# Optimization experiments

Hardware: AMD Instinct MI355X
Metric: run time of the kernel (lower is better)

The kernel has to match this reference:

```python
import jax, jax.numpy as jnp
import numpy as np

B, T, D = 4, 2048, 1024
E = 16            # routed experts
S = 2             # shared experts
MOE_TOPK = 2
COSINE_LAMBDA = 0.1


def setup_inputs() -> dict:
    key = jax.random.key(0)
    k_x, k_g, k_sh, k_rt = jax.random.split(key, 4)
    x = jax.random.normal(k_x, (B, T, D), dtype=jnp.float32)
    gate_w = jax.random.normal(k_g, (E, D), dtype=jnp.float32) * 0.02
    gate_b = jnp.zeros((E,), dtype=jnp.float32)
    shared_experts = jax.random.normal(k_sh, (S, D), dtype=jnp.float32) * 0.1
    routed_experts = jax.random.normal(k_rt, (E, D), dtype=jnp.float32) * 0.1
    return {"x": x, "gate_w": gate_w, "gate_b": gate_b,
            "shared_experts": shared_experts, "routed_experts": routed_experts}


def reference(x, gate_w, gate_b, shared_experts, routed_experts):
    b, t, d = x.shape
    n = b * t
    hidden = x.reshape(n, d)                                   # [N, D]

    # ---- router ----
    logits = hidden @ gate_w.T + gate_b                        # [N, E]
    probs = jax.nn.softmax(logits, axis=-1)                    # stable (shift-invariant)
    topk_vals, topk_idx = jax.lax.top_k(probs, MOE_TOPK)       # [N, K]
    if MOE_TOPK == 1:
        weights = jnp.ones_like(topk_vals)
    else:
        weights = topk_vals / jnp.clip(topk_vals.sum(-1, keepdims=True), 1e-6)

    # ---- shared experts (always active): sum_e hidden * w_e ----
    shared_sum = hidden * shared_experts.sum(0)                # [N, D]

    # ---- dense all-expert elementwise scale (as in original) ----
    routed_outs = hidden[None, :, :] * routed_experts[:, None, :]   # [E, N, D]

    # ---- diversity loss: cosine sim between flattened expert outputs ----
    flat = routed_outs.reshape(E, -1)                          # [E, N*D]
    norms = jnp.maximum(jnp.linalg.norm(flat, axis=1, keepdims=True), 1e-8)
    normed = flat / norms
    sim = jnp.clip(normed @ normed.T, -1.0, 1.0)               # [E, E]
    mask = 1.0 - jnp.eye(E, dtype=sim.dtype)
    div_loss = (sim * mask).sum() / max(E * (E - 1), 1) * COSINE_LAMBDA

    # ---- top-k gather + weighted combine ----
    routed_nd = routed_outs.transpose(1, 0, 2)                 # [N, E, D]
    sel = jnp.take_along_axis(routed_nd, topk_idx[:, :, None], axis=1)  # [N, K, D]
    dyn_sum = (sel * weights[:, :, None]).sum(axis=1)          # [N, D]

    out = (shared_sum + dyn_sum).reshape(b, t, d)
    return out, div_loss
```

## Files before the change

kernel.cpp:

```cpp
#include <hip/hip_runtime.h>

#define NTOK 8192
#define DDIM 1024
#define NEXP 16
#define NPAIR 136
#define XROW 1032
#define NBLK 2048
#define NRED 64

#define WS_GWT  0
#define WS_SLOT 16384
#define WS_GP   (WS_SLOT + NBLK * DDIM)

__global__ __launch_bounds__(256) void moe_prep(
    const float* __restrict__ gate_w,
    float* __restrict__ ws)
{
    const int gid = blockIdx.x * 256 + threadIdx.x;
    const int e = gid & 15;
    const int d4 = gid >> 4;
    const float4* gw4 = (const float4*)gate_w;
    float4* gwT4 = (float4*)(ws + WS_GWT);
    gwT4[d4 * 16 + e] = gw4[e * 256 + d4];
}

__global__ __launch_bounds__(256, 8) void moe_fused(
    const float* __restrict__ x,
    const float* __restrict__ gate_b,
    const float* __restrict__ sh,
    const float* __restrict__ re,
    float* __restrict__ out,
    float* __restrict__ ws)
{
    __shared__ __align__(16) float xt[4][XROW];

    const int t = threadIdx.x;
    const int b = blockIdx.x;
    const float4* gwT4 = (const float4*)(ws + WS_GWT);

    float4 ss = make_float4(0.f, 0.f, 0.f, 0.f);
    {
        const float4* x4 = (const float4*)x + (size_t)b * 1024;
        #pragma unroll
        for (int i = 0; i < 4; ++i) {
            float4 v = x4[i * 256 + t];
            *(float4*)&xt[i][4 * t] = v;
            ss.x = fmaf(v.x, v.x, ss.x);
            ss.y = fmaf(v.y, v.y, ss.y);
            ss.z = fmaf(v.z, v.z, ss.z);
            ss.w = fmaf(v.w, v.w, ss.w);
        }
    }
    __syncthreads();

    const int lane = t & 63;
    const int wv = t >> 6;
    const int e = lane & 15;
    const int qr = lane >> 4;

    const float* xrow = &xt[wv][qr * 256];
    const float4* gt = gwT4 + qr * 64 * 16;
    float4 a4 = make_float4(0.f, 0.f, 0.f, 0.f);
    #pragma unroll 8
    for (int i = 0; i < 64; ++i) {
        float4 xv = *(const float4*)(xrow + 4 * i);
        float4 gv = gt[i * 16 + e];
        a4.x = fmaf(xv.x, gv.x, a4.x);
        a4.y = fmaf(xv.y, gv.y, a4.y);
        a4.z = fmaf(xv.z, gv.z, a4.z);
        a4.w = fmaf(xv.w, gv.w, a4.w);
    }
    float acc = (a4.x + a4.y) + (a4.z + a4.w);
    acc += __shfl_xor(acc, 16, 64);
    acc += __shfl_xor(acc, 32, 64);
    acc += gate_b[e];

    float v0 = -3.0e38f, v1 = -3.0e38f;
    int i0 = 0, i1 = 0;
    const int base = lane & 48;
    #pragma unroll
    for (int j = 0; j < NEXP; ++j) {
        float lv = __shfl(acc, base + j, 64);
        if (lv > v0)      { v1 = v0; i1 = i0; v0 = lv; i0 = j; }
        else if (lv > v1) { v1 = lv; i1 = j; }
    }
    float ex = __expf(v1 - v0);
    float w0 = 1.f / (1.f + ex);
    float w1 = ex * w0;

    float4 shs[4];
    {
        const float4* s0 = (const float4*)sh;
        const float4* s1 = (const float4*)(sh + DDIM);
        #pragma unroll
        for (int j = 0; j < 4; ++j) {
            float4 p = s0[lane + 64 * j];
            float4 s = s1[lane + 64 * j];
            shs[j] = make_float4(p.x + s.x, p.y + s.y, p.z + s.z, p.w + s.w);
        }
    }

    {
        const float4* xr = (const float4*)&xt[wv][0];
        const float4* r0 = (const float4*)(re + (size_t)i0 * DDIM);
        const float4* r1 = (const float4*)(re + (size_t)i1 * DDIM);
        float4* o = (float4*)(out + ((size_t)b * 4 + wv) * DDIM);
        #pragma unroll
        for (int j = 0; j < 4; ++j) {
            const int idx = lane + 64 * j;
            float4 xv = xr[idx];
            float4 b0 = r0[idx];
            float4 b1 = r1[idx];
            float4 r;
            r.x = xv.x * (shs[j].x + w0 * b0.x + w1 * b1.x);
            r.y = xv.y * (shs[j].y + w0 * b0.y + w1 * b1.y);
            r.z = xv.z * (shs[j].z + w0 * b0.z + w1 * b1.z);
            r.w = xv.w * (shs[j].w + w0 * b0.w + w1 * b1.w);
            o[idx] = r;
        }
    }

    *(float4*)(ws + WS_SLOT + (size_t)b * DDIM + 4 * t) = ss;
}

__global__ __launch_bounds__(256) void moe_xred_gram(
    const float* __restrict__ re,
    float* __restrict__ ws)
{
    __shared__ float4 s4[64][4];
    __shared__ float s_loc[16];
    __shared__ float reT[16][16];

    const int t = threadIdx.x;
    const int j = blockIdx.x;
    const int c = t & 3;
    const int r = t >> 2;

    {
        const float4* sl4 = (const float4*)(ws + WS_SLOT);
        const size_t colbase = (size_t)4 * j + c;
        float4 acc = make_float4(0.f, 0.f, 0.f, 0.f);
        #pragma unroll 8
        for (int k = 0; k < 32; ++k) {
            float4 v = sl4[(size_t)(r + 64 * k) * 256 + colbase];
            acc.x += v.x; acc.y += v.y; acc.z += v.z; acc.w += v.w;
        }
        s4[r][c] = acc;
    }
    {
        const int e = t >> 4, dd = t & 15;
        reT[dd][e] = re[(size_t)e * DDIM + 16 * j + dd];
    }
    __syncthreads();

    if (t < 4) {
        float4 a = s4[0][t];
        for (int rr = 1; rr < 64; ++rr) {
            float4 v = s4[rr][t];
            a.x += v.x; a.y += v.y; a.z += v.z; a.w += v.w;
        }
        s_loc[4 * t + 0] = a.x;
        s_loc[4 * t + 1] = a.y;
        s_loc[4 * t + 2] = a.z;
        s_loc[4 * t + 3] = a.w;
    }
    __syncthreads();

    if (t < NPAIR) {
        int pe = 0, rem = t;
        while (rem >= NEXP - pe) { rem -= NEXP - pe; ++pe; }
        const int pf = pe + rem;
        float a = 0.f;
        #pragma unroll
        for (int dd = 0; dd < 16; ++dd)
            a += s_loc[dd] * reT[dd][pe] * reT[dd][pf];
        (ws + WS_GP)[j * NPAIR + t] = a;
    }
}

__global__ __launch_bounds__(192) void moe_final(
    const float* __restrict__ ws,
    float* __restrict__ div_out)
{
    __shared__ float G[NPAIR];
    __shared__ float nr[NEXP];
    __shared__ float lsum;
    const int t = threadIdx.x;

    if (t == 0) lsum = 0.f;
    if (t < NPAIR) {
        const float* gp = ws + WS_GP;
        float g = 0.f;
        #pragma unroll 8
        for (int jj = 0; jj < NRED; ++jj) g += gp[jj * NPAIR + t];
        G[t] = g;
    }
    __syncthreads();
    if (t < NEXP) {
        int idx = t * NEXP - (t * (t - 1)) / 2;
        nr[t] = fmaxf(sqrtf(G[idx]), 1e-8f);
    }
    __syncthreads();
    if (t < NPAIR) {
        int pe = 0, rem = t;
        while (rem >= NEXP - pe) { rem -= NEXP - pe; ++pe; }
        const int pf = pe + rem;
        if (pe != pf) {
            float sim = G[t] / (nr[pe] * nr[pf]);
            sim = fminf(1.f, fmaxf(-1.f, sim));
            atomicAdd(&lsum, 2.f * sim);
        }
    }
    __syncthreads();
    if (t == 0) *div_out = lsum / (float)(NEXP * (NEXP - 1)) * 0.1f;
}

extern "C" void kernel_launch(void* const* d_in, const int* in_sizes, int n_in,
                              void* d_out, int out_size, void* d_ws, size_t ws_size,
                              hipStream_t stream) {
    const float* x  = (const float*)d_in[0];
    const float* gw = (const float*)d_in[1];
    const float* gb = (const float*)d_in[2];
    const float* sh = (const float*)d_in[3];
    const float* re = (const float*)d_in[4];
    float* out = (float*)d_out;
    float* ws = (float*)d_ws;

    moe_prep<<<16, 256, 0, stream>>>(gw, ws);
    moe_fused<<<NBLK, 256, 0, stream>>>(x, gb, sh, re, out, ws);
    moe_xred_gram<<<NRED, 256, 0, stream>>>(re, ws);
    moe_final<<<1, 192, 0, stream>>>(ws, out + (size_t)NTOK * DDIM);
}
```

Before: 130.0 us.

## Fuse final reduction into gram kernel via last-block counter and pad LDS rows

Removes the separate single-block final kernel: each gram block atomically stores its partials, increments a counter, and the last block reads all partials under an acquire fence and computes the diversity loss. The shared-memory x tile is padded per quarter row, adding 8 floats after each 256, to reduce LDS bank conflicts in the router dot product. The sum-of-squares store is also moved before the barrier. This saves one kernel launch but adds an atomic counter and fence, and relies on the prep kernel resetting the counter on every call.

Measured after the change: 141.7 us. +9.0%, slower.

```diff
diff --git a/kernel.cpp b/kernel.cpp
--- a/kernel.cpp
+++ b/kernel.cpp
@@ -4,13 +4,14 @@
 #define DDIM 1024
 #define NEXP 16
 #define NPAIR 136
-#define XROW 1032
+#define QPAD 264
 #define NBLK 2048
 #define NRED 64
 
 #define WS_GWT  0
 #define WS_SLOT 16384
 #define WS_GP   (WS_SLOT + NBLK * DDIM)
+#define WS_CNT  (WS_GP + NRED * NPAIR)
 
 __global__ __launch_bounds__(256) void moe_prep(
     const float* __restrict__ gate_w,
@@ -22,6 +23,7 @@
     const float4* gw4 = (const float4*)gate_w;
     float4* gwT4 = (float4*)(ws + WS_GWT);
     gwT4[d4 * 16 + e] = gw4[e * 256 + d4];
+    if (gid == 0) ((int*)ws)[WS_CNT] = 0;
 }
 
 __global__ __launch_bounds__(256, 8) void moe_fused(
@@ -32,7 +34,7 @@
     float* __restrict__ out,
     float* __restrict__ ws)
 {
-    __shared__ __align__(16) float xt[4][XROW];
+    __shared__ __align__(16) float xt[4][4 * QPAD];
 
     const int t = threadIdx.x;
     const int b = blockIdx.x;
@@ -41,16 +43,18 @@
     float4 ss = make_float4(0.f, 0.f, 0.f, 0.f);
     {
         const float4* x4 = (const float4*)x + (size_t)b * 1024;
+        const int dst = 4 * t + 8 * (t >> 6);
         #pragma unroll
         for (int i = 0; i < 4; ++i) {
             float4 v = x4[i * 256 + t];
-            *(float4*)&xt[i][4 * t] = v;
+            *(float4*)&xt[i][dst] = v;
             ss.x = fmaf(v.x, v.x, ss.x);
             ss.y = fmaf(v.y, v.y, ss.y);
             ss.z = fmaf(v.z, v.z, ss.z);
             ss.w = fmaf(v.w, v.w, ss.w);
         }
     }
+    *(float4*)(ws + WS_SLOT + (size_t)b * DDIM + 4 * t) = ss;
     __syncthreads();
 
     const int lane = t & 63;
@@ -58,7 +62,7 @@
     const int e = lane & 15;
     const int qr = lane >> 4;
 
-    const float* xrow = &xt[wv][qr * 256];
+    const float* xrow = &xt[wv][qr * QPAD];
     const float4* gt = gwT4 + qr * 64 * 16;
     float4 a4 = make_float4(0.f, 0.f, 0.f, 0.f);
     #pragma unroll 8
@@ -101,14 +105,13 @@
     }
 
     {
-        const float4* xr = (const float4*)&xt[wv][0];
         const float4* r0 = (const float4*)(re + (size_t)i0 * DDIM);
         const float4* r1 = (const float4*)(re + (size_t)i1 * DDIM);
         float4* o = (float4*)(out + ((size_t)b * 4 + wv) * DDIM);
         #pragma unroll
         for (int j = 0; j < 4; ++j) {
             const int idx = lane + 64 * j;
-            float4 xv = xr[idx];
+            float4 xv = ((const float4*)&xt[wv][j * QPAD])[lane];
             float4 b0 = r0[idx];
             float4 b1 = r1[idx];
             float4 r;
@@ -119,22 +122,26 @@
             o[idx] = r;
         }
     }
-
-    *(float4*)(ws + WS_SLOT + (size_t)b * DDIM + 4 * t) = ss;
 }
 
 __global__ __launch_bounds__(256) void moe_xred_gram(
     const float* __restrict__ re,
-    float* __restrict__ ws)
+    float* __restrict__ ws,
+    float* __restrict__ div_out)
 {
     __shared__ float4 s4[64][4];
     __shared__ float s_loc[16];
     __shared__ float reT[16][16];
+    __shared__ float Gs[NPAIR];
+    __shared__ float nr[NEXP];
+    __shared__ float lsum;
+    __shared__ int   role;
 
     const int t = threadIdx.x;
     const int j = blockIdx.x;
     const int c = t & 3;
     const int r = t >> 2;
+    int* cnt = (int*)ws + WS_CNT;
 
     {
         const float4* sl4 = (const float4*)(ws + WS_SLOT);
@@ -174,18 +181,18 @@
         #pragma unroll
         for (int dd = 0; dd < 16; ++dd)
             a += s_loc[dd] * reT[dd][pe] * reT[dd][pf];
-        (ws + WS_GP)[j * NPAIR + t] = a;
-    }
-}
-
-__global__ __launch_bounds__(192) void moe_final(
-    const float* __restrict__ ws,
-    float* __restrict__ div_out)
-{
-    __shared__ float G[NPAIR];
-    __shared__ float nr[NEXP];
-    __shared__ float lsum;
-    const int t = threadIdx.x;
+        __hip_atomic_store(ws + WS_GP + j * NPAIR + t, a,
+                           __ATOMIC_RELAXED, __HIP_MEMORY_SCOPE_AGENT);
+    }
+
+    __syncthreads();
+    if (t == 0) {
+        int k = atomicAdd(cnt, 1);
+        role = (k == NRED - 1);
+    }
+    __syncthreads();
+    if (!role) return;
+    __builtin_amdgcn_fence(__ATOMIC_ACQUIRE, "agent");
 
     if (t == 0) lsum = 0.f;
     if (t < NPAIR) {
@@ -193,12 +200,12 @@
         float g = 0.f;
         #pragma unroll 8
         for (int jj = 0; jj < NRED; ++jj) g += gp[jj * NPAIR + t];
-        G[t] = g;
+        Gs[t] = g;
     }
     __syncthreads();
     if (t < NEXP) {
         int idx = t * NEXP - (t * (t - 1)) / 2;
-        nr[t] = fmaxf(sqrtf(G[idx]), 1e-8f);
+        nr[t] = fmaxf(sqrtf(Gs[idx]), 1e-8f);
     }
     __syncthreads();
     if (t < NPAIR) {
@@ -206,7 +213,7 @@
         while (rem >= NEXP - pe) { rem -= NEXP - pe; ++pe; }
         const int pf = pe + rem;
         if (pe != pf) {
-            float sim = G[t] / (nr[pe] * nr[pf]);
+            float sim = Gs[t] / (nr[pe] * nr[pf]);
             sim = fminf(1.f, fmaxf(-1.f, sim));
             atomicAdd(&lsum, 2.f * sim);
         }
@@ -228,6 +235,5 @@
 
     moe_prep<<<16, 256, 0, stream>>>(gw, ws);
     moe_fused<<<NBLK, 256, 0, stream>>>(x, gb, sh, re, out, ws);
-    moe_xred_gram<<<NRED, 256, 0, stream>>>(re, ws);
-    moe_final<<<1, 192, 0, stream>>>(ws, out + (size_t)NTOK * DDIM);
-}
+    moe_xred_gram<<<NRED, 256, 0, stream>>>(re, ws, out + (size_t)NTOK * DDIM);
+}
```

## Restructure router GEMV to reuse gate weights across four tokens and drop transpose kernel

Applied to the files above, without the earlier changes.

The separate gate-weight transpose kernel is removed. Each wave now reads gate_w rows directly and applies each loaded weight vector to four tokens, so the four waves split the D dimension. Partial logits are combined through a small shared-memory array and an extra barrier. The x tile in shared memory gets a padded layout with staggered iteration order to reduce bank conflicts. The cost is the extra sync and LDS round trip, plus more registers for four accumulators.

Result: slower. 134.4 us (+3.4%).

```diff
diff --git a/kernel.cpp b/kernel.cpp
--- a/kernel.cpp
+++ b/kernel.cpp
@@ -4,47 +4,36 @@
 #define DDIM 1024
 #define NEXP 16
 #define NPAIR 136
-#define XROW 1032
+#define QPAD 264
 #define NBLK 2048
 #define NRED 64
 
-#define WS_GWT  0
-#define WS_SLOT 16384
-#define WS_GP   (WS_SLOT + NBLK * DDIM)
-
-__global__ __launch_bounds__(256) void moe_prep(
-    const float* __restrict__ gate_w,
-    float* __restrict__ ws)
-{
-    const int gid = blockIdx.x * 256 + threadIdx.x;
-    const int e = gid & 15;
-    const int d4 = gid >> 4;
-    const float4* gw4 = (const float4*)gate_w;
-    float4* gwT4 = (float4*)(ws + WS_GWT);
-    gwT4[d4 * 16 + e] = gw4[e * 256 + d4];
-}
+#define WS_SLOT 0
+#define WS_GP   (NBLK * DDIM)
 
 __global__ __launch_bounds__(256, 8) void moe_fused(
     const float* __restrict__ x,
+    const float* __restrict__ gate_w,
     const float* __restrict__ gate_b,
     const float* __restrict__ sh,
     const float* __restrict__ re,
     float* __restrict__ out,
     float* __restrict__ ws)
 {
-    __shared__ __align__(16) float xt[4][XROW];
+    __shared__ __align__(16) float xt[4][4 * QPAD];
+    __shared__ float lg[4][4][16];
 
     const int t = threadIdx.x;
     const int b = blockIdx.x;
-    const float4* gwT4 = (const float4*)(ws + WS_GWT);
 
     float4 ss = make_float4(0.f, 0.f, 0.f, 0.f);
     {
         const float4* x4 = (const float4*)x + (size_t)b * 1024;
+        const int dst = 4 * t + 8 * (t >> 6);
         #pragma unroll
         for (int i = 0; i < 4; ++i) {
             float4 v = x4[i * 256 + t];
-            *(float4*)&xt[i][4 * t] = v;
+            *(float4*)&xt[i][dst] = v;
             ss.x = fmaf(v.x, v.x, ss.x);
             ss.y = fmaf(v.y, v.y, ss.y);
             ss.z = fmaf(v.z, v.z, ss.z);
@@ -56,33 +45,55 @@
     const int lane = t & 63;
     const int wv = t >> 6;
     const int e = lane & 15;
-    const int qr = lane >> 4;
-
-    const float* xrow = &xt[wv][qr * 256];
-    const float4* gt = gwT4 + qr * 64 * 16;
-    float4 a4 = make_float4(0.f, 0.f, 0.f, 0.f);
-    #pragma unroll 8
-    for (int i = 0; i < 64; ++i) {
-        float4 xv = *(const float4*)(xrow + 4 * i);
-        float4 gv = gt[i * 16 + e];
-        a4.x = fmaf(xv.x, gv.x, a4.x);
-        a4.y = fmaf(xv.y, gv.y, a4.y);
-        a4.z = fmaf(xv.z, gv.z, a4.z);
-        a4.w = fmaf(xv.w, gv.w, a4.w);
-    }
-    float acc = (a4.x + a4.y) + (a4.z + a4.w);
-    acc += __shfl_xor(acc, 16, 64);
-    acc += __shfl_xor(acc, 32, 64);
-    acc += gate_b[e];
+    const int sub = lane >> 4;
+
+    const float4* gt = (const float4*)gate_w + (size_t)e * 256 + wv * 64 + sub * 16;
+    const float* xq = &xt[0][wv * QPAD + sub * 64];
+    float4 a0 = make_float4(0.f, 0.f, 0.f, 0.f), a1 = a0, a2 = a0, a3 = a0;
+    #pragma unroll
+    for (int ii = 0; ii < 16; ++ii) {
+        const int i = (ii + 2 * sub) & 15;
+        float4 gv = gt[i];
+        const float* xp = xq + 4 * i;
+        float4 x0 = *(const float4*)(xp);
+        float4 x1 = *(const float4*)(xp + 4 * QPAD);
+        float4 x2 = *(const float4*)(xp + 8 * QPAD);
+        float4 x3 = *(const float4*)(xp + 12 * QPAD);
+        a0.x = fmaf(gv.x, x0.x, a0.x); a0.y = fmaf(gv.y, x0.y, a0.y);
+        a0.z = fmaf(gv.z, x0.z, a0.z); a0.w = fmaf(gv.w, x0.w, a0.w);
+        a1.x = fmaf(gv.x, x1.x, a1.x); a1.y = fmaf(gv.y, x1.y, a1.y);
+        a1.z = fmaf(gv.z, x1.z, a1.z); a1.w = fmaf(gv.w, x1.w, a1.w);
+        a2.x = fmaf(gv.x, x2.x, a2.x); a2.y = fmaf(gv.y, x2.y, a2.y);
+        a2.z = fmaf(gv.z, x2.z, a2.z); a2.w = fmaf(gv.w, x2.w, a2.w);
+        a3.x = fmaf(gv.x, x3.x, a3.x); a3.y = fmaf(gv.y, x3.y, a3.y);
+        a3.z = fmaf(gv.z, x3.z, a3.z); a3.w = fmaf(gv.w, x3.w, a3.w);
+    }
+    float r0 = (a0.x + a0.y) + (a0.z + a0.w);
+    float r1 = (a1.x + a1.y) + (a1.z + a1.w);
+    float r2 = (a2.x + a2.y) + (a2.z + a2.w);
+    float r3 = (a3.x + a3.y) + (a3.z + a3.w);
+    r0 += __shfl_xor(r0, 16, 64); r0 += __shfl_xor(r0, 32, 64);
+    r1 += __shfl_xor(r1, 16, 64); r1 += __shfl_xor(r1, 32, 64);
+    r2 += __shfl_xor(r2, 16, 64); r2 += __shfl_xor(r2, 32, 64);
+    r3 += __shfl_xor(r3, 16, 64); r3 += __shfl_xor(r3, 32, 64);
+    if (lane < 16) {
+        lg[0][wv][lane] = r0;
+        lg[1][wv][lane] = r1;
+        lg[2][wv][lane] = r2;
+        lg[3][wv][lane] = r3;
+    }
+    __syncthreads();
+    float lv = ((lg[wv][0][e] + lg[wv][1][e]) + (lg[wv][2][e] + lg[wv][3][e]))
+             + gate_b[e];
 
     float v0 = -3.0e38f, v1 = -3.0e38f;
     int i0 = 0, i1 = 0;
     const int base = lane & 48;
     #pragma unroll
     for (int j = 0; j < NEXP; ++j) {
-        float lv = __shfl(acc, base + j, 64);
-        if (lv > v0)      { v1 = v0; i1 = i0; v0 = lv; i0 = j; }
-        else if (lv > v1) { v1 = lv; i1 = j; }
+        float lj = __shfl(lv, base + j, 64);
+        if (lj > v0)      { v1 = v0; i1 = i0; v0 = lj; i0 = j; }
+        else if (lj > v1) { v1 = lj; i1 = j; }
     }
     float ex = __expf(v1 - v0);
     float w0 = 1.f / (1.f + ex);
@@ -101,16 +112,15 @@
     }
 
     {
-        const float4* xr = (const float4*)&xt[wv][0];
-        const float4* r0 = (const float4*)(re + (size_t)i0 * DDIM);
-        const float4* r1 = (const float4*)(re + (size_t)i1 * DDIM);
+        const float4* r0p = (const float4*)(re + (size_t)i0 * DDIM);
+        const float4* r1p = (const float4*)(re + (size_t)i1 * DDIM);
         float4* o = (float4*)(out + ((size_t)b * 4 + wv) * DDIM);
         #pragma unroll
         for (int j = 0; j < 4; ++j) {
             const int idx = lane + 64 * j;
-            float4 xv = xr[idx];
-            float4 b0 = r0[idx];
-            float4 b1 = r1[idx];
+            float4 xv = ((const float4*)&xt[wv][j * QPAD])[lane];
+            float4 b0 = r0p[idx];
+            float4 b1 = r1p[idx];
             float4 r;
             r.x = xv.x * (shs[j].x + w0 * b0.x + w1 * b1.x);
             r.y = xv.y * (shs[j].y + w0 * b0.y + w1 * b1.y);
@@ -226,8 +236,7 @@
     float* out = (float*)d_out;
     float* ws = (float*)d_ws;
 
-    moe_prep<<<16, 256, 0, stream>>>(gw, ws);
-    moe_fused<<<NBLK, 256, 0, stream>>>(x, gb, sh, re, out, ws);
+    moe_fused<<<NBLK, 256, 0, stream>>>(x, gw, gb, sh, re, out, ws);
     moe_xred_gram<<<NRED, 256, 0, stream>>>(re, ws);
     moe_final<<<1, 192, 0, stream>>>(ws, out + (size_t)NTOK * DDIM);
 }
```
